# Kernel tuning notes

Measured on AMD Instinct MI355X. Metric: run time of the kernel, lower is better.

Reference implementation:

```python
import jax, jax.numpy as jnp
import numpy as np

N = 50000      # nodes
E = 800000     # edges
IN = 16        # embedding_dimension
HID = 128      # hidden_dimension
OUT = 3        # out_dim
R = 2          # relation_num
NEG_SLOPE = 0.2  # PyG RGATConv default negative_slope


def setup_inputs() -> dict:
    key = jax.random.key(0)
    ks = jax.random.split(key, 9)
    feature = jax.random.normal(ks[0], (N, IN), jnp.float32)
    edge_index = jax.random.randint(ks[1], (2, E), 0, N, jnp.int32)
    edge_type = jax.random.randint(ks[2], (E,), 0, R, jnp.int32)
    # RGATConv params (heads=1): weight [R, in, out], q/k [out, 1], bias [out]
    W1 = jax.random.normal(ks[3], (R, IN, HID), jnp.float32) * (1.0 / np.sqrt(IN))
    q1 = jax.random.normal(ks[4], (HID, 1), jnp.float32) * (1.0 / np.sqrt(HID))
    k1 = jax.random.normal(ks[5], (HID, 1), jnp.float32) * (1.0 / np.sqrt(HID))
    b1 = jnp.zeros((HID,), jnp.float32)
    W2 = jax.random.normal(ks[6], (R, HID, OUT), jnp.float32) * (1.0 / np.sqrt(HID))
    q2 = jax.random.normal(ks[7], (OUT, 1), jnp.float32) * (1.0 / np.sqrt(OUT))
    k2 = jax.random.normal(ks[8], (OUT, 1), jnp.float32) * (1.0 / np.sqrt(OUT))
    b2 = jnp.zeros((OUT,), jnp.float32)
    return dict(feature=feature, edge_index=edge_index, edge_type=edge_type,
                W1=W1, q1=q1, k1=k1, b1=b1, W2=W2, q2=q2, k2=k2, b2=b2)


def rgat_conv(x, src, dst, edge_type, W, q, k, b, n_nodes):
    # Per-relation node transform once at node level: [R, N, C]
    # (equivalent to per-edge bmm with W[edge_type] in PyG, but avoids
    #  gathering [E, in, C] weight matrices)
    xr = jnp.einsum('nd,rdc->rnc', x, W)
    out_i = xr[edge_type, dst]  # target node transformed by edge relation, [E, C]
    out_j = xr[edge_type, src]  # source node transformed by edge relation, [E, C]
    # additive self-attention, heads=1: alpha = leaky_relu(q(x_i) + k(x_j))
    alpha = jax.nn.leaky_relu((out_i @ q + out_j @ k)[:, 0], NEG_SLOPE)  # [E]
    # across-relation softmax over incoming edges of each target node
    m = jax.ops.segment_max(alpha, dst, num_segments=n_nodes)
    ex = jnp.exp(alpha - m[dst])
    denom = jax.ops.segment_sum(ex, dst, num_segments=n_nodes)
    a = ex / (denom[dst] + 1e-16)
    # message = alpha * W_r x_j, scatter-sum to target nodes
    out = jax.ops.segment_sum(out_j * a[:, None], dst, num_segments=n_nodes)
    return out + b


def reference(feature, edge_index, edge_type, W1, q1, k1, b1, W2, q2, k2, b2):
    src, dst = edge_index[0], edge_index[1]  # PyG: row 0 = source j, row 1 = target i
    h = rgat_conv(feature, src, dst, edge_type, W1, q1, k1, b1, N)
    # F.dropout(p=0.3) is identity in eval mode
    out = rgat_conv(h, src, dst, edge_type, W2, q2, k2, b2, N)
    return out
```

## Files before the change

### kernel.cpp

```cpp
#include <hip/hip_runtime.h>
#include <math.h>

#define IN_DIM 16
#define HID 128
#define NEG 0.2f
#define ABLK 8192
#define CAP 4608

__device__ __forceinline__ float lrelu(float a) { return a > 0.f ? a : NEG * a; }

__global__ void __launch_bounds__(256) k_pre(
    const float* __restrict__ W1, const float* __restrict__ q1, const float* __restrict__ k1,
    const float* __restrict__ b1, const float* __restrict__ W2, const float* __restrict__ q2,
    const float* __restrict__ k2,
    float* __restrict__ wq1, float* __restrict__ wk1,
    float* __restrict__ M, float* __restrict__ C,
    int* __restrict__ gCursor, int nbkt) {
    int zi = blockIdx.x * 256 + threadIdx.x;
    if (zi < nbkt) gCursor[zi] = 0;

    int w = blockIdx.x * 4 + (threadIdx.x >> 6);
    if (w >= 362) return;
    int lane = threadIdx.x & 63;

    auto T = [&](int c, int o) -> float {
        if (o < 3) return W2[c * 3 + o];
        if (o < 6) return W2[384 + c * 3 + (o - 3)];
        const float* base = (o == 6 || o == 8) ? (W2 + c * 3) : (W2 + 384 + c * 3);
        const float* v = (o < 8) ? q2 : k2;
        return base[0] * v[0] + base[1] * v[1] + base[2] * v[2];
    };

    if (w < 330) {
        bool isC = (w >= 320);
        int o  = isC ? (w - 320) : (w % 10);
        int dp = isC ? 0 : (w / 10);
        float acc = 0.f;
        for (int c = lane; c < HID; c += 64) {
            float left = isC ? b1[c] : W1[dp * HID + c];
            acc += left * T(c, o);
        }
#pragma unroll
        for (int off = 32; off; off >>= 1) acc += __shfl_xor(acc, off);
        if (lane == 0) { if (isC) C[o] = acc; else M[dp * 10 + o] = acc; }
    } else {
        int i = w - 330;
        float aq = 0.f, ak = 0.f;
        for (int c = lane; c < HID; c += 64) {
            float wv = W1[i * HID + c];
            aq += wv * q1[c]; ak += wv * k1[c];
        }
#pragma unroll
        for (int off = 32; off; off >>= 1) { aq += __shfl_xor(aq, off); ak += __shfl_xor(ak, off); }
        if (lane == 0) { wq1[i] = aq; wk1[i] = ak; }
    }
}

__global__ void __launch_bounds__(256) k_bin(
    const int* __restrict__ srcp, const int* __restrict__ dstp,
    const int* __restrict__ etp,
    int* __restrict__ gCursor, int* __restrict__ binned,
    const float* __restrict__ x,
    const float* __restrict__ wq1, const float* __restrict__ wk1,
    float* __restrict__ sq1, float* __restrict__ sk1,
    int n_nodes, int ecnt, int nbkt) {
    __shared__ int lh[256];
    __shared__ int runB[256];
    __shared__ float wq[2 * IN_DIM], wk[2 * IN_DIM];
    int t = threadIdx.x;
    lh[t] = 0;
    if (t < 2 * IN_DIM) { wq[t] = wq1[t]; wk[t] = wk1[t]; }
    __syncthreads();
    int E0 = blockIdx.x * ABLK;
    int rb[ABLK / 256];
#pragma unroll
    for (int k = 0; k < ABLK / 256; ++k) {
        int e = E0 + k * 256 + t;
        int v = -1;
        if (e < ecnt) {
            int b = dstp[e] >> 8;
            int r = atomicAdd(&lh[b], 1);
            v = (r << 8) | b;
        }
        rb[k] = v;
    }
    __syncthreads();
    if (t < nbkt && lh[t]) runB[t] = atomicAdd(&gCursor[t], lh[t]);
    __syncthreads();
#pragma unroll
    for (int k = 0; k < ABLK / 256; ++k) {
        int v = rb[k];
        if (v < 0) continue;
        int b = v & 255, r = v >> 8;
        int e = E0 + k * 256 + t;
        binned[b * CAP + runB[b] + r] = ((dstp[e] & 255) << 17) | (etp[e] << 16) | srcp[e];
    }
    int stride = gridDim.x * 256;
    for (int n = blockIdx.x * 256 + t; n < n_nodes; n += stride) {
        float q0 = 0.f, q1v = 0.f, k0 = 0.f, k1v = 0.f;
        const float4* xp = reinterpret_cast<const float4*>(x + (size_t)n * IN_DIM);
#pragma unroll
        for (int d4 = 0; d4 < IN_DIM / 4; ++d4) {
            float4 v = xp[d4];
            float vv[4] = {v.x, v.y, v.z, v.w};
#pragma unroll
            for (int j = 0; j < 4; ++j) {
                int d = d4 * 4 + j;
                q0 += vv[j] * wq[d]; q1v += vv[j] * wq[IN_DIM + d];
                k0 += vv[j] * wk[d]; k1v += vv[j] * wk[IN_DIM + d];
            }
        }
        sq1[n] = q0; sq1[n_nodes + n] = q1v;
        sk1[n] = k0; sk1[n_nodes + n] = k1v;
    }
}

__global__ void __launch_bounds__(256) k_build(
    const int* __restrict__ gCursor, const int* __restrict__ binned,
    int* __restrict__ offsets, int* __restrict__ sorted,
    int n_nodes, int ecnt, int nbkt) {
    __shared__ int ss[256], lh[256], loff[256], lcur[256];
    int t = threadIdx.x, b = blockIdx.x;
    int gv = (t < nbkt) ? gCursor[t] : 0;
    ss[t] = gv;
    lh[t] = 0;
    __syncthreads();
    for (int off = 1; off < 256; off <<= 1) {
        int u = (t >= off) ? ss[t - off] : 0;
        __syncthreads();
        ss[t] += u;
        __syncthreads();
    }
    int sz = gCursor[b];
    int myStart = ss[b] - sz;
    __syncthreads();
    for (int i = t; i < sz; i += 256) {
        int v = binned[b * CAP + i];
        atomicAdd(&lh[(v >> 17) & 255], 1);
    }
    __syncthreads();
    ss[t] = lh[t];
    __syncthreads();
    for (int off = 1; off < 256; off <<= 1) {
        int u = (t >= off) ? ss[t - off] : 0;
        __syncthreads();
        ss[t] += u;
        __syncthreads();
    }
    loff[t] = ss[t] - lh[t];
    lcur[t] = 0;
    __syncthreads();
    int node = b * 256 + t;
    if (node < n_nodes) offsets[node] = myStart + loff[t];
    if (b == nbkt - 1 && t == 0) offsets[n_nodes] = ecnt;
    for (int i = t; i < sz; i += 256) {
        int v = binned[b * CAP + i];
        int dl = (v >> 17) & 255;
        int p = loff[dl] + atomicAdd(&lcur[dl], 1);
        sorted[myStart + p] = v & 0x1FFFF;
    }
}

__global__ void __launch_bounds__(256) k_layer1(
    const int* __restrict__ offsets, const int* __restrict__ sorted,
    const float* __restrict__ sq1, const float* __restrict__ sk1,
    const float* __restrict__ x, const float* __restrict__ M, const float* __restrict__ C,
    float* __restrict__ xr2p, float* __restrict__ sq2,
    int n_nodes) {
    __shared__ float Ml[320], Cl[10];
    __shared__ float Al[4][32];
    for (int i = threadIdx.x; i < 320; i += 256) Ml[i] = M[i];
    if (threadIdx.x < 10)  Cl[threadIdx.x] = C[threadIdx.x];
    __syncthreads();
    int wid = threadIdx.x >> 6, lane = threadIdx.x & 63;
    int n = blockIdx.x * 4 + wid;
    if (n >= n_nodes) return;
    int beg = offsets[n], end = offsets[n + 1];
    float s0 = sq1[n], s1 = sq1[n_nodes + n];
    int ch4 = lane & 3, j = lane >> 2;
    float4 a0 = make_float4(0.f, 0.f, 0.f, 0.f);
    float4 a1 = make_float4(0.f, 0.f, 0.f, 0.f);
    float ds = 0.f;
    const float4* x4 = reinterpret_cast<const float4*>(x);
    for (int e = beg + j; e < end; e += 16) {
        int pk = sorted[e];
        int et = pk >> 16, s = pk & 0xFFFF;
        float w = __expf(lrelu((et ? s1 : s0) + sk1[et * n_nodes + s]));
        ds += w;
        float4 xv = x4[s * 4 + ch4];
        if (et == 0) { a0.x += w * xv.x; a0.y += w * xv.y; a0.z += w * xv.z; a0.w += w * xv.w; }
        else         { a1.x += w * xv.x; a1.y += w * xv.y; a1.z += w * xv.z; a1.w += w * xv.w; }
    }
#pragma unroll
    for (int off = 4; off <= 32; off <<= 1) {
        a0.x += __shfl_xor(a0.x, off); a0.y += __shfl_xor(a0.y, off);
        a0.z += __shfl_xor(a0.z, off); a0.w += __shfl_xor(a0.w, off);
        a1.x += __shfl_xor(a1.x, off); a1.y += __shfl_xor(a1.y, off);
        a1.z += __shfl_xor(a1.z, off); a1.w += __shfl_xor(a1.w, off);
        ds += __shfl_xor(ds, off);
    }
    float inv = 1.f / (ds + 1e-16f);
    if (lane < 4) {
        reinterpret_cast<float4*>(&Al[wid][0])[lane] =
            make_float4(a0.x * inv, a0.y * inv, a0.z * inv, a0.w * inv);
        reinterpret_cast<float4*>(&Al[wid][16])[lane] =
            make_float4(a1.x * inv, a1.y * inv, a1.z * inv, a1.w * inv);
    }
    if (lane < 10) {
        float acc = Cl[lane];
#pragma unroll
        for (int dp = 0; dp < 32; ++dp) acc += Al[wid][dp] * Ml[dp * 10 + lane];
        int o = lane;
        if (o < 3)       xr2p[(size_t)n * 4 + o] = acc;
        else if (o < 6)  xr2p[((size_t)n_nodes + n) * 4 + (o - 3)] = acc;
        else if (o == 6) sq2[2 * n] = acc;
        else if (o == 7) sq2[2 * n + 1] = acc;
        else if (o == 8) xr2p[(size_t)n * 4 + 3] = acc;
        else             xr2p[((size_t)n_nodes + n) * 4 + 3] = acc;
    }
}

__global__ void __launch_bounds__(256) k_node2(
    const int* __restrict__ offsets, const int* __restrict__ sorted,
    const float* __restrict__ sq2, const float* __restrict__ xr2p,
    const float* __restrict__ b2, float* __restrict__ out,
    int n_nodes) {
    int gid = blockIdx.x * 256 + threadIdx.x;
    int n = gid >> 4;
    int l = threadIdx.x & 15;
    if (n >= n_nodes) return;
    int beg = offsets[n], end = offsets[n + 1];
    if (beg == end) {
        if (l < 3) out[(size_t)n * 3 + l] = b2[l];
        return;
    }
    const float2 sq = *reinterpret_cast<const float2*>(sq2 + 2 * n);
    float lsum = 0.f, a0 = 0.f, a1 = 0.f, a2 = 0.f;
    for (int e = beg + l; e < end; e += 16) {
        int pk = sorted[e];
        int et = pk >> 16, s = pk & 0xFFFF;
        const float4 xr = *reinterpret_cast<const float4*>(xr2p + ((size_t)et * n_nodes + s) * 4);
        float w = __expf(lrelu((et ? sq.y : sq.x) + xr.w));
        lsum += w;
        a0 += w * xr.x; a1 += w * xr.y; a2 += w * xr.z;
    }
#pragma unroll
    for (int off = 8; off; off >>= 1) {
        lsum += __shfl_xor(lsum, off);
        a0 += __shfl_xor(a0, off);
        a1 += __shfl_xor(a1, off);
        a2 += __shfl_xor(a2, off);
    }
    if (l == 0) {
        float inv = 1.f / (lsum + 1e-16f);
        out[(size_t)n * 3 + 0] = a0 * inv + b2[0];
        out[(size_t)n * 3 + 1] = a1 * inv + b2[1];
        out[(size_t)n * 3 + 2] = a2 * inv + b2[2];
    }
}

extern "C" void kernel_launch(void* const* d_in, const int* in_sizes, int n_in,
                              void* d_out, int out_size, void* d_ws, size_t ws_size,
                              hipStream_t stream) {
    const float* x  = (const float*)d_in[0];
    const int*   ei = (const int*)d_in[1];
    const int*   etp = (const int*)d_in[2];
    const float* W1 = (const float*)d_in[3];
    const float* q1 = (const float*)d_in[4];
    const float* k1 = (const float*)d_in[5];
    const float* b1 = (const float*)d_in[6];
    const float* W2 = (const float*)d_in[7];
    const float* q2 = (const float*)d_in[8];
    const float* k2 = (const float*)d_in[9];
    const float* b2 = (const float*)d_in[10];
    float* out = (float*)d_out;

    const int n_nodes = in_sizes[0] / IN_DIM;
    const int ecnt    = in_sizes[2];
    const int* srcp = ei;
    const int* dstp = ei + ecnt;
    const int nbkt = (n_nodes + 255) >> 8;

    char* wp = (char*)d_ws;
    auto alloc = [&](size_t bytes) -> char* {
        char* p = wp;
        wp += (bytes + 255) & ~(size_t)255;
        return p;
    };
    float* xr2p  = (float*)alloc((size_t)2 * n_nodes * 4 * 4);
    float* sq1   = (float*)alloc((size_t)2 * n_nodes * 4);
    float* sk1   = (float*)alloc((size_t)2 * n_nodes * 4);
    float* sq2   = (float*)alloc((size_t)2 * n_nodes * 4);
    float* wq1   = (float*)alloc(32 * 4);
    float* wk1   = (float*)alloc(32 * 4);
    float* Mbuf  = (float*)alloc(320 * 4);
    float* Cbuf  = (float*)alloc(10 * 4);
    int* gCursor = (int*)alloc(256 * 4);
    int* offsets = (int*)alloc((size_t)(n_nodes + 1) * 4);
    int* binned  = (int*)alloc((size_t)nbkt * CAP * 4);
    int* sorted  = (int*)alloc((size_t)ecnt * 4);

    int nAblk = (ecnt + ABLK - 1) / ABLK;

    k_pre<<<91, 256, 0, stream>>>(W1, q1, k1, b1, W2, q2, k2, wq1, wk1, Mbuf, Cbuf,
                                  gCursor, nbkt);
    k_bin<<<nAblk, 256, 0, stream>>>(srcp, dstp, etp, gCursor, binned,
                                     x, wq1, wk1, sq1, sk1, n_nodes, ecnt, nbkt);
    k_build<<<nbkt, 256, 0, stream>>>(gCursor, binned, offsets, sorted, n_nodes, ecnt, nbkt);

    k_layer1<<<(n_nodes + 3) / 4, 256, 0, stream>>>(offsets, sorted, sq1, sk1, x, Mbuf, Cbuf,
                                                    xr2p, sq2, n_nodes);
    k_node2<<<(n_nodes * 16 + 255) / 256, 256, 0, stream>>>(offsets, sorted, sq2, xr2p, b2,
                                                            out, n_nodes);
}
```

Measured before the change: 93.39 us.

## Drop CSR build; aggregate per-bucket edges with shared-memory atomics

Removes the k_build counting-sort pass and the offsets/sorted arrays. Both layers now aggregate directly from the per-bucket binned edge lists, one 1024-thread block per 256-node bucket, and accumulate into shared-memory arrays with atomics. Layer 1 also applies the 16x10 projection matrix M per edge before accumulating, so it stores 11 accumulators per node instead of 32 features. This saves a kernel launch and a global scatter pass, at the cost of shared-atomic contention, more per-edge arithmetic, and only about 196 blocks, which is low parallelism.

```diff
diff --git a/kernel.cpp b/kernel.cpp
--- a/kernel.cpp
+++ b/kernel.cpp
@@ -115,147 +115,100 @@
     }
 }
 
-__global__ void __launch_bounds__(256) k_build(
+__global__ void __launch_bounds__(1024) k_agg1(
     const int* __restrict__ gCursor, const int* __restrict__ binned,
-    int* __restrict__ offsets, int* __restrict__ sorted,
-    int n_nodes, int ecnt, int nbkt) {
-    __shared__ int ss[256], lh[256], loff[256], lcur[256];
-    int t = threadIdx.x, b = blockIdx.x;
-    int gv = (t < nbkt) ? gCursor[t] : 0;
-    ss[t] = gv;
-    lh[t] = 0;
-    __syncthreads();
-    for (int off = 1; off < 256; off <<= 1) {
-        int u = (t >= off) ? ss[t - off] : 0;
-        __syncthreads();
-        ss[t] += u;
-        __syncthreads();
-    }
-    int sz = gCursor[b];
-    int myStart = ss[b] - sz;
-    __syncthreads();
-    for (int i = t; i < sz; i += 256) {
-        int v = binned[b * CAP + i];
-        atomicAdd(&lh[(v >> 17) & 255], 1);
-    }
-    __syncthreads();
-    ss[t] = lh[t];
-    __syncthreads();
-    for (int off = 1; off < 256; off <<= 1) {
-        int u = (t >= off) ? ss[t - off] : 0;
-        __syncthreads();
-        ss[t] += u;
-        __syncthreads();
-    }
-    loff[t] = ss[t] - lh[t];
-    lcur[t] = 0;
-    __syncthreads();
-    int node = b * 256 + t;
-    if (node < n_nodes) offsets[node] = myStart + loff[t];
-    if (b == nbkt - 1 && t == 0) offsets[n_nodes] = ecnt;
-    for (int i = t; i < sz; i += 256) {
-        int v = binned[b * CAP + i];
-        int dl = (v >> 17) & 255;
-        int p = loff[dl] + atomicAdd(&lcur[dl], 1);
-        sorted[myStart + p] = v & 0x1FFFF;
-    }
-}
-
-__global__ void __launch_bounds__(256) k_layer1(
-    const int* __restrict__ offsets, const int* __restrict__ sorted,
     const float* __restrict__ sq1, const float* __restrict__ sk1,
     const float* __restrict__ x, const float* __restrict__ M, const float* __restrict__ C,
-    float* __restrict__ xr2p, float* __restrict__ sq2,
-    int n_nodes) {
+    float* __restrict__ xr2p, float* __restrict__ sq2, int n_nodes) {
     __shared__ float Ml[320], Cl[10];
-    __shared__ float Al[4][32];
-    for (int i = threadIdx.x; i < 320; i += 256) Ml[i] = M[i];
-    if (threadIdx.x < 10)  Cl[threadIdx.x] = C[threadIdx.x];
-    __syncthreads();
-    int wid = threadIdx.x >> 6, lane = threadIdx.x & 63;
-    int n = blockIdx.x * 4 + wid;
-    if (n >= n_nodes) return;
-    int beg = offsets[n], end = offsets[n + 1];
-    float s0 = sq1[n], s1 = sq1[n_nodes + n];
-    int ch4 = lane & 3, j = lane >> 2;
-    float4 a0 = make_float4(0.f, 0.f, 0.f, 0.f);
-    float4 a1 = make_float4(0.f, 0.f, 0.f, 0.f);
-    float ds = 0.f;
+    __shared__ float sql[2][256];
+    __shared__ float acc[256][13];
+    int t = threadIdx.x, b = blockIdx.x;
+    for (int i = t; i < 320; i += 1024) Ml[i] = M[i];
+    if (t < 10) Cl[t] = C[t];
+    int nbase = b << 8;
+    if (t < 512) {
+        int r = t >> 8, dl = t & 255;
+        int n = nbase + dl;
+        sql[r][dl] = (n < n_nodes) ? sq1[r * n_nodes + n] : 0.f;
+    }
+    for (int i = t; i < 256 * 13; i += 1024) (&acc[0][0])[i] = 0.f;
+    __syncthreads();
+    int sz = gCursor[b];
     const float4* x4 = reinterpret_cast<const float4*>(x);
-    for (int e = beg + j; e < end; e += 16) {
-        int pk = sorted[e];
-        int et = pk >> 16, s = pk & 0xFFFF;
-        float w = __expf(lrelu((et ? s1 : s0) + sk1[et * n_nodes + s]));
-        ds += w;
-        float4 xv = x4[s * 4 + ch4];
-        if (et == 0) { a0.x += w * xv.x; a0.y += w * xv.y; a0.z += w * xv.z; a0.w += w * xv.w; }
-        else         { a1.x += w * xv.x; a1.y += w * xv.y; a1.z += w * xv.z; a1.w += w * xv.w; }
-    }
-#pragma unroll
-    for (int off = 4; off <= 32; off <<= 1) {
-        a0.x += __shfl_xor(a0.x, off); a0.y += __shfl_xor(a0.y, off);
-        a0.z += __shfl_xor(a0.z, off); a0.w += __shfl_xor(a0.w, off);
-        a1.x += __shfl_xor(a1.x, off); a1.y += __shfl_xor(a1.y, off);
-        a1.z += __shfl_xor(a1.z, off); a1.w += __shfl_xor(a1.w, off);
-        ds += __shfl_xor(ds, off);
-    }
-    float inv = 1.f / (ds + 1e-16f);
-    if (lane < 4) {
-        reinterpret_cast<float4*>(&Al[wid][0])[lane] =
-            make_float4(a0.x * inv, a0.y * inv, a0.z * inv, a0.w * inv);
-        reinterpret_cast<float4*>(&Al[wid][16])[lane] =
-            make_float4(a1.x * inv, a1.y * inv, a1.z * inv, a1.w * inv);
-    }
-    if (lane < 10) {
-        float acc = Cl[lane];
-#pragma unroll
-        for (int dp = 0; dp < 32; ++dp) acc += Al[wid][dp] * Ml[dp * 10 + lane];
-        int o = lane;
-        if (o < 3)       xr2p[(size_t)n * 4 + o] = acc;
-        else if (o < 6)  xr2p[((size_t)n_nodes + n) * 4 + (o - 3)] = acc;
-        else if (o == 6) sq2[2 * n] = acc;
-        else if (o == 7) sq2[2 * n + 1] = acc;
-        else if (o == 8) xr2p[(size_t)n * 4 + 3] = acc;
-        else             xr2p[((size_t)n_nodes + n) * 4 + 3] = acc;
-    }
-}
-
-__global__ void __launch_bounds__(256) k_node2(
-    const int* __restrict__ offsets, const int* __restrict__ sorted,
+    for (int i = t; i < sz; i += 1024) {
+        int v = binned[b * CAP + i];
+        int dl = (v >> 17) & 255, et = (v >> 16) & 1, s = v & 0xFFFF;
+        float w = __expf(lrelu(sql[et][dl] + sk1[et * n_nodes + s]));
+        float4 xa = x4[s * 4 + 0], xb = x4[s * 4 + 1];
+        float4 xc = x4[s * 4 + 2], xd = x4[s * 4 + 3];
+        float xv[16] = {xa.x, xa.y, xa.z, xa.w, xb.x, xb.y, xb.z, xb.w,
+                        xc.x, xc.y, xc.z, xc.w, xd.x, xd.y, xd.z, xd.w};
+        const float* Mr = &Ml[et * 160];
+        float* ab = acc[dl];
+#pragma unroll
+        for (int o = 0; o < 10; ++o) {
+            float a = 0.f;
+#pragma unroll
+            for (int dd = 0; dd < 16; ++dd) a += xv[dd] * Mr[dd * 10 + o];
+            atomicAdd(&ab[o], w * a);
+        }
+        atomicAdd(&ab[10], w);
+    }
+    __syncthreads();
+    if (t < 256) {
+        int n = nbase + t;
+        if (n < n_nodes) {
+            float inv = 1.f / (acc[t][10] + 1e-16f);
+            float o[10];
+#pragma unroll
+            for (int i = 0; i < 10; ++i) o[i] = acc[t][i] * inv + Cl[i];
+            reinterpret_cast<float4*>(xr2p)[n]           = make_float4(o[0], o[1], o[2], o[8]);
+            reinterpret_cast<float4*>(xr2p)[n_nodes + n] = make_float4(o[3], o[4], o[5], o[9]);
+            reinterpret_cast<float2*>(sq2)[n]            = make_float2(o[6], o[7]);
+        }
+    }
+}
+
+__global__ void __launch_bounds__(1024) k_agg2(
+    const int* __restrict__ gCursor, const int* __restrict__ binned,
     const float* __restrict__ sq2, const float* __restrict__ xr2p,
-    const float* __restrict__ b2, float* __restrict__ out,
-    int n_nodes) {
-    int gid = blockIdx.x * 256 + threadIdx.x;
-    int n = gid >> 4;
-    int l = threadIdx.x & 15;
-    if (n >= n_nodes) return;
-    int beg = offsets[n], end = offsets[n + 1];
-    if (beg == end) {
-        if (l < 3) out[(size_t)n * 3 + l] = b2[l];
-        return;
-    }
-    const float2 sq = *reinterpret_cast<const float2*>(sq2 + 2 * n);
-    float lsum = 0.f, a0 = 0.f, a1 = 0.f, a2 = 0.f;
-    for (int e = beg + l; e < end; e += 16) {
-        int pk = sorted[e];
-        int et = pk >> 16, s = pk & 0xFFFF;
-        const float4 xr = *reinterpret_cast<const float4*>(xr2p + ((size_t)et * n_nodes + s) * 4);
-        float w = __expf(lrelu((et ? sq.y : sq.x) + xr.w));
-        lsum += w;
-        a0 += w * xr.x; a1 += w * xr.y; a2 += w * xr.z;
-    }
-#pragma unroll
-    for (int off = 8; off; off >>= 1) {
-        lsum += __shfl_xor(lsum, off);
-        a0 += __shfl_xor(a0, off);
-        a1 += __shfl_xor(a1, off);
-        a2 += __shfl_xor(a2, off);
-    }
-    if (l == 0) {
-        float inv = 1.f / (lsum + 1e-16f);
-        out[(size_t)n * 3 + 0] = a0 * inv + b2[0];
-        out[(size_t)n * 3 + 1] = a1 * inv + b2[1];
-        out[(size_t)n * 3 + 2] = a2 * inv + b2[2];
+    const float* __restrict__ b2, float* __restrict__ out, int n_nodes) {
+    __shared__ float sql[256][2];
+    __shared__ float acc[256][5];
+    __shared__ float b2l[3];
+    int t = threadIdx.x, b = blockIdx.x;
+    if (t < 3) b2l[t] = b2[t];
+    int nbase = b << 8;
+    if (t < 256) {
+        int n = nbase + t;
+        float2 s = (n < n_nodes) ? reinterpret_cast<const float2*>(sq2)[n]
+                                 : make_float2(0.f, 0.f);
+        sql[t][0] = s.x; sql[t][1] = s.y;
+        acc[t][0] = acc[t][1] = acc[t][2] = acc[t][3] = 0.f;
+    }
+    __syncthreads();
+    int sz = gCursor[b];
+    for (int i = t; i < sz; i += 1024) {
+        int v = binned[b * CAP + i];
+        int dl = (v >> 17) & 255, et = (v >> 16) & 1, s = v & 0xFFFF;
+        float4 xr = reinterpret_cast<const float4*>(xr2p)[(size_t)et * n_nodes + s];
+        float w = __expf(lrelu(sql[dl][et] + xr.w));
+        float* ab = acc[dl];
+        atomicAdd(&ab[0], w * xr.x);
+        atomicAdd(&ab[1], w * xr.y);
+        atomicAdd(&ab[2], w * xr.z);
+        atomicAdd(&ab[3], w);
+    }
+    __syncthreads();
+    if (t < 256) {
+        int n = nbase + t;
+        if (n < n_nodes) {
+            float inv = 1.f / (acc[t][3] + 1e-16f);
+            out[(size_t)n * 3 + 0] = acc[t][0] * inv + b2l[0];
+            out[(size_t)n * 3 + 1] = acc[t][1] * inv + b2l[1];
+            out[(size_t)n * 3 + 2] = acc[t][2] * inv + b2l[2];
+        }
     }
 }
 
@@ -296,9 +249,7 @@
     float* Mbuf  = (float*)alloc(320 * 4);
     float* Cbuf  = (float*)alloc(10 * 4);
     int* gCursor = (int*)alloc(256 * 4);
-    int* offsets = (int*)alloc((size_t)(n_nodes + 1) * 4);
     int* binned  = (int*)alloc((size_t)nbkt * CAP * 4);
-    int* sorted  = (int*)alloc((size_t)ecnt * 4);
 
     int nAblk = (ecnt + ABLK - 1) / ABLK;
 
@@ -306,10 +257,7 @@
                                   gCursor, nbkt);
     k_bin<<<nAblk, 256, 0, stream>>>(srcp, dstp, etp, gCursor, binned,
                                      x, wq1, wk1, sq1, sk1, n_nodes, ecnt, nbkt);
-    k_build<<<nbkt, 256, 0, stream>>>(gCursor, binned, offsets, sorted, n_nodes, ecnt, nbkt);
-
-    k_layer1<<<(n_nodes + 3) / 4, 256, 0, stream>>>(offsets, sorted, sq1, sk1, x, Mbuf, Cbuf,
-                                                    xr2p, sq2, n_nodes);
-    k_node2<<<(n_nodes * 16 + 255) / 256, 256, 0, stream>>>(offsets, sorted, sq2, xr2p, b2,
-                                                            out, n_nodes);
-}
+    k_agg1<<<nbkt, 1024, 0, stream>>>(gCursor, binned, sq1, sk1, x, Mbuf, Cbuf,
+                                      xr2p, sq2, n_nodes);
+    k_agg2<<<nbkt, 1024, 0, stream>>>(gCursor, binned, sq2, xr2p, b2, out, n_nodes);
+}
```

Result: slower. 131.3 us (+40.6%).

## Fuse CSR build into layer kernels using per-bucket shared-memory sort

Applied to the files above, without the earlier changes.

Removes the separate k_build kernel and the global offsets/sorted arrays. Each layer kernel now runs one 1024-thread block per 256-node bucket, counting-sorts that bucket's binned edges into shared memory, then processes its nodes from LDS. This saves a kernel launch and the global write and read-back of the sorted edge list. In exchange the sort is done twice (once per layer), only 196 blocks are launched on a large GPU, and each block uses a lot of LDS, which may hurt parallelism and latency hiding.

```diff
diff --git a/kernel.cpp b/kernel.cpp
--- a/kernel.cpp
+++ b/kernel.cpp
@@ -115,147 +115,157 @@
     }
 }
 
-__global__ void __launch_bounds__(256) k_build(
+__global__ void __launch_bounds__(1024) k_l1(
     const int* __restrict__ gCursor, const int* __restrict__ binned,
-    int* __restrict__ offsets, int* __restrict__ sorted,
-    int n_nodes, int ecnt, int nbkt) {
-    __shared__ int ss[256], lh[256], loff[256], lcur[256];
+    const float* __restrict__ sq1, const float* __restrict__ sk1,
+    const float* __restrict__ x, const float* __restrict__ M, const float* __restrict__ C,
+    float* __restrict__ xr2p, float* __restrict__ sq2, int n_nodes) {
+    __shared__ float Ml[320], Cl[10];
+    __shared__ int lh[256], loff[256], lcur[256], ss[256];
+    __shared__ int sortedL[CAP];
+    __shared__ float Al[16][32];
     int t = threadIdx.x, b = blockIdx.x;
-    int gv = (t < nbkt) ? gCursor[t] : 0;
-    ss[t] = gv;
-    lh[t] = 0;
+    int nbase = b << 8;
+    for (int i = t; i < 320; i += 1024) Ml[i] = M[i];
+    if (t < 10) Cl[t] = C[t];
+    if (t < 256) { lh[t] = 0; lcur[t] = 0; }
+    __syncthreads();
+    int sz = gCursor[b];
+    for (int i = t; i < sz; i += 1024)
+        atomicAdd(&lh[(binned[b * CAP + i] >> 17) & 255], 1);
+    __syncthreads();
+    if (t < 256) ss[t] = lh[t];
     __syncthreads();
     for (int off = 1; off < 256; off <<= 1) {
-        int u = (t >= off) ? ss[t - off] : 0;
+        int u = (t >= off && t < 256) ? ss[t - off] : 0;
         __syncthreads();
-        ss[t] += u;
+        if (t < 256) ss[t] += u;
         __syncthreads();
     }
-    int sz = gCursor[b];
-    int myStart = ss[b] - sz;
-    __syncthreads();
-    for (int i = t; i < sz; i += 256) {
-        int v = binned[b * CAP + i];
-        atomicAdd(&lh[(v >> 17) & 255], 1);
-    }
-    __syncthreads();
-    ss[t] = lh[t];
-    __syncthreads();
-    for (int off = 1; off < 256; off <<= 1) {
-        int u = (t >= off) ? ss[t - off] : 0;
-        __syncthreads();
-        ss[t] += u;
-        __syncthreads();
-    }
-    loff[t] = ss[t] - lh[t];
-    lcur[t] = 0;
-    __syncthreads();
-    int node = b * 256 + t;
-    if (node < n_nodes) offsets[node] = myStart + loff[t];
-    if (b == nbkt - 1 && t == 0) offsets[n_nodes] = ecnt;
-    for (int i = t; i < sz; i += 256) {
+    if (t < 256) loff[t] = ss[t] - lh[t];
+    __syncthreads();
+    for (int i = t; i < sz; i += 1024) {
         int v = binned[b * CAP + i];
         int dl = (v >> 17) & 255;
         int p = loff[dl] + atomicAdd(&lcur[dl], 1);
-        sorted[myStart + p] = v & 0x1FFFF;
-    }
-}
-
-__global__ void __launch_bounds__(256) k_layer1(
-    const int* __restrict__ offsets, const int* __restrict__ sorted,
-    const float* __restrict__ sq1, const float* __restrict__ sk1,
-    const float* __restrict__ x, const float* __restrict__ M, const float* __restrict__ C,
-    float* __restrict__ xr2p, float* __restrict__ sq2,
-    int n_nodes) {
-    __shared__ float Ml[320], Cl[10];
-    __shared__ float Al[4][32];
-    for (int i = threadIdx.x; i < 320; i += 256) Ml[i] = M[i];
-    if (threadIdx.x < 10)  Cl[threadIdx.x] = C[threadIdx.x];
-    __syncthreads();
-    int wid = threadIdx.x >> 6, lane = threadIdx.x & 63;
-    int n = blockIdx.x * 4 + wid;
-    if (n >= n_nodes) return;
-    int beg = offsets[n], end = offsets[n + 1];
-    float s0 = sq1[n], s1 = sq1[n_nodes + n];
+        sortedL[p] = v & 0x1FFFF;
+    }
+    __syncthreads();
+    int wid = t >> 6, lane = t & 63;
     int ch4 = lane & 3, j = lane >> 2;
-    float4 a0 = make_float4(0.f, 0.f, 0.f, 0.f);
-    float4 a1 = make_float4(0.f, 0.f, 0.f, 0.f);
-    float ds = 0.f;
     const float4* x4 = reinterpret_cast<const float4*>(x);
-    for (int e = beg + j; e < end; e += 16) {
-        int pk = sorted[e];
-        int et = pk >> 16, s = pk & 0xFFFF;
-        float w = __expf(lrelu((et ? s1 : s0) + sk1[et * n_nodes + s]));
-        ds += w;
-        float4 xv = x4[s * 4 + ch4];
-        if (et == 0) { a0.x += w * xv.x; a0.y += w * xv.y; a0.z += w * xv.z; a0.w += w * xv.w; }
-        else         { a1.x += w * xv.x; a1.y += w * xv.y; a1.z += w * xv.z; a1.w += w * xv.w; }
-    }
-#pragma unroll
-    for (int off = 4; off <= 32; off <<= 1) {
-        a0.x += __shfl_xor(a0.x, off); a0.y += __shfl_xor(a0.y, off);
-        a0.z += __shfl_xor(a0.z, off); a0.w += __shfl_xor(a0.w, off);
-        a1.x += __shfl_xor(a1.x, off); a1.y += __shfl_xor(a1.y, off);
-        a1.z += __shfl_xor(a1.z, off); a1.w += __shfl_xor(a1.w, off);
-        ds += __shfl_xor(ds, off);
-    }
-    float inv = 1.f / (ds + 1e-16f);
-    if (lane < 4) {
-        reinterpret_cast<float4*>(&Al[wid][0])[lane] =
-            make_float4(a0.x * inv, a0.y * inv, a0.z * inv, a0.w * inv);
-        reinterpret_cast<float4*>(&Al[wid][16])[lane] =
-            make_float4(a1.x * inv, a1.y * inv, a1.z * inv, a1.w * inv);
-    }
-    if (lane < 10) {
-        float acc = Cl[lane];
-#pragma unroll
-        for (int dp = 0; dp < 32; ++dp) acc += Al[wid][dp] * Ml[dp * 10 + lane];
-        int o = lane;
-        if (o < 3)       xr2p[(size_t)n * 4 + o] = acc;
-        else if (o < 6)  xr2p[((size_t)n_nodes + n) * 4 + (o - 3)] = acc;
-        else if (o == 6) sq2[2 * n] = acc;
-        else if (o == 7) sq2[2 * n + 1] = acc;
-        else if (o == 8) xr2p[(size_t)n * 4 + 3] = acc;
-        else             xr2p[((size_t)n_nodes + n) * 4 + 3] = acc;
-    }
-}
-
-__global__ void __launch_bounds__(256) k_node2(
-    const int* __restrict__ offsets, const int* __restrict__ sorted,
+    for (int g = 0; g < 16; ++g) {
+        int dl = wid * 16 + g;
+        int n = nbase + dl;
+        if (n >= n_nodes) continue;
+        int beg = loff[dl], end = beg + lh[dl];
+        float s0 = sq1[n], s1 = sq1[n_nodes + n];
+        float4 a0 = make_float4(0.f, 0.f, 0.f, 0.f);
+        float4 a1 = make_float4(0.f, 0.f, 0.f, 0.f);
+        float ds = 0.f;
+        for (int e = beg + j; e < end; e += 16) {
+            int pk = sortedL[e];
+            int et = pk >> 16, s = pk & 0xFFFF;
+            float w = __expf(lrelu((et ? s1 : s0) + sk1[et * n_nodes + s]));
+            ds += w;
+            float4 xv = x4[s * 4 + ch4];
+            if (et == 0) { a0.x += w * xv.x; a0.y += w * xv.y; a0.z += w * xv.z; a0.w += w * xv.w; }
+            else         { a1.x += w * xv.x; a1.y += w * xv.y; a1.z += w * xv.z; a1.w += w * xv.w; }
+        }
+#pragma unroll
+        for (int off = 4; off <= 32; off <<= 1) {
+            a0.x += __shfl_xor(a0.x, off); a0.y += __shfl_xor(a0.y, off);
+            a0.z += __shfl_xor(a0.z, off); a0.w += __shfl_xor(a0.w, off);
+            a1.x += __shfl_xor(a1.x, off); a1.y += __shfl_xor(a1.y, off);
+            a1.z += __shfl_xor(a1.z, off); a1.w += __shfl_xor(a1.w, off);
+            ds += __shfl_xor(ds, off);
+        }
+        float inv = 1.f / (ds + 1e-16f);
+        if (lane < 4) {
+            reinterpret_cast<float4*>(&Al[wid][0])[lane] =
+                make_float4(a0.x * inv, a0.y * inv, a0.z * inv, a0.w * inv);
+            reinterpret_cast<float4*>(&Al[wid][16])[lane] =
+                make_float4(a1.x * inv, a1.y * inv, a1.z * inv, a1.w * inv);
+        }
+        if (lane < 10) {
+            float acc = Cl[lane];
+#pragma unroll
+            for (int dp = 0; dp < 32; ++dp) acc += Al[wid][dp] * Ml[dp * 10 + lane];
+            int o = lane;
+            if (o < 3)       xr2p[(size_t)n * 4 + o] = acc;
+            else if (o < 6)  xr2p[((size_t)n_nodes + n) * 4 + (o - 3)] = acc;
+            else if (o == 6) sq2[2 * n] = acc;
+            else if (o == 7) sq2[2 * n + 1] = acc;
+            else if (o == 8) xr2p[(size_t)n * 4 + 3] = acc;
+            else             xr2p[((size_t)n_nodes + n) * 4 + 3] = acc;
+        }
+    }
+}
+
+__global__ void __launch_bounds__(1024) k_l2(
+    const int* __restrict__ gCursor, const int* __restrict__ binned,
     const float* __restrict__ sq2, const float* __restrict__ xr2p,
-    const float* __restrict__ b2, float* __restrict__ out,
-    int n_nodes) {
-    int gid = blockIdx.x * 256 + threadIdx.x;
-    int n = gid >> 4;
-    int l = threadIdx.x & 15;
-    if (n >= n_nodes) return;
-    int beg = offsets[n], end = offsets[n + 1];
-    if (beg == end) {
-        if (l < 3) out[(size_t)n * 3 + l] = b2[l];
-        return;
-    }
-    const float2 sq = *reinterpret_cast<const float2*>(sq2 + 2 * n);
-    float lsum = 0.f, a0 = 0.f, a1 = 0.f, a2 = 0.f;
-    for (int e = beg + l; e < end; e += 16) {
-        int pk = sorted[e];
-        int et = pk >> 16, s = pk & 0xFFFF;
-        const float4 xr = *reinterpret_cast<const float4*>(xr2p + ((size_t)et * n_nodes + s) * 4);
-        float w = __expf(lrelu((et ? sq.y : sq.x) + xr.w));
-        lsum += w;
-        a0 += w * xr.x; a1 += w * xr.y; a2 += w * xr.z;
-    }
-#pragma unroll
-    for (int off = 8; off; off >>= 1) {
-        lsum += __shfl_xor(lsum, off);
-        a0 += __shfl_xor(a0, off);
-        a1 += __shfl_xor(a1, off);
-        a2 += __shfl_xor(a2, off);
-    }
-    if (l == 0) {
-        float inv = 1.f / (lsum + 1e-16f);
-        out[(size_t)n * 3 + 0] = a0 * inv + b2[0];
-        out[(size_t)n * 3 + 1] = a1 * inv + b2[1];
-        out[(size_t)n * 3 + 2] = a2 * inv + b2[2];
+    const float* __restrict__ b2, float* __restrict__ out, int n_nodes) {
+    __shared__ int lh[256], loff[256], lcur[256], ss[256];
+    __shared__ int sortedL[CAP];
+    __shared__ float b2l[3];
+    int t = threadIdx.x, b = blockIdx.x;
+    int nbase = b << 8;
+    if (t < 3) b2l[t] = b2[t];
+    if (t < 256) { lh[t] = 0; lcur[t] = 0; }
+    __syncthreads();
+    int sz = gCursor[b];
+    for (int i = t; i < sz; i += 1024)
+        atomicAdd(&lh[(binned[b * CAP + i] >> 17) & 255], 1);
+    __syncthreads();
+    if (t < 256) ss[t] = lh[t];
+    __syncthreads();
+    for (int off = 1; off < 256; off <<= 1) {
+        int u = (t >= off && t < 256) ? ss[t - off] : 0;
+        __syncthreads();
+        if (t < 256) ss[t] += u;
+        __syncthreads();
+    }
+    if (t < 256) loff[t] = ss[t] - lh[t];
+    __syncthreads();
+    for (int i = t; i < sz; i += 1024) {
+        int v = binned[b * CAP + i];
+        int dl = (v >> 17) & 255;
+        int p = loff[dl] + atomicAdd(&lcur[dl], 1);
+        sortedL[p] = v & 0x1FFFF;
+    }
+    __syncthreads();
+    int wid = t >> 6, lane = t & 63;
+    int l = lane & 15;
+    const float4* xr4 = reinterpret_cast<const float4*>(xr2p);
+    for (int g = 0; g < 4; ++g) {
+        int dl = wid * 16 + g * 4 + (lane >> 4);
+        int n = nbase + dl;
+        bool valid = (n < n_nodes);
+        int beg = loff[dl], end = beg + lh[dl];
+        float2 sq = valid ? reinterpret_cast<const float2*>(sq2)[n] : make_float2(0.f, 0.f);
+        float lsum = 0.f, a0 = 0.f, a1 = 0.f, a2 = 0.f;
+        for (int e = beg + l; e < end; e += 16) {
+            int pk = sortedL[e];
+            int et = pk >> 16, s = pk & 0xFFFF;
+            float4 xr = xr4[(size_t)et * n_nodes + s];
+            float w = __expf(lrelu((et ? sq.y : sq.x) + xr.w));
+            lsum += w;
+            a0 += w * xr.x; a1 += w * xr.y; a2 += w * xr.z;
+        }
+#pragma unroll
+        for (int off = 8; off; off >>= 1) {
+            lsum += __shfl_xor(lsum, off);
+            a0 += __shfl_xor(a0, off);
+            a1 += __shfl_xor(a1, off);
+            a2 += __shfl_xor(a2, off);
+        }
+        if (l == 0 && valid) {
+            float inv = 1.f / (lsum + 1e-16f);
+            out[(size_t)n * 3 + 0] = a0 * inv + b2l[0];
+            out[(size_t)n * 3 + 1] = a1 * inv + b2l[1];
+            out[(size_t)n * 3 + 2] = a2 * inv + b2l[2];
+        }
     }
 }
 
@@ -296,9 +306,7 @@
     float* Mbuf  = (float*)alloc(320 * 4);
     float* Cbuf  = (float*)alloc(10 * 4);
     int* gCursor = (int*)alloc(256 * 4);
-    int* offsets = (int*)alloc((size_t)(n_nodes + 1) * 4);
     int* binned  = (int*)alloc((size_t)nbkt * CAP * 4);
-    int* sorted  = (int*)alloc((size_t)ecnt * 4);
 
     int nAblk = (ecnt + ABLK - 1) / ABLK;
 
@@ -306,10 +314,7 @@
                                   gCursor, nbkt);
     k_bin<<<nAblk, 256, 0, stream>>>(srcp, dstp, etp, gCursor, binned,
                                      x, wq1, wk1, sq1, sk1, n_nodes, ecnt, nbkt);
-    k_build<<<nbkt, 256, 0, stream>>>(gCursor, binned, offsets, sorted, n_nodes, ecnt, nbkt);
-
-    k_layer1<<<(n_nodes + 3) / 4, 256, 0, stream>>>(offsets, sorted, sq1, sk1, x, Mbuf, Cbuf,
-                                                    xr2p, sq2, n_nodes);
-    k_node2<<<(n_nodes * 16 + 255) / 256, 256, 0, stream>>>(offsets, sorted, sq2, xr2p, b2,
-                                                            out, n_nodes);
-}
+    k_l1<<<nbkt, 1024, 0, stream>>>(gCursor, binned, sq1, sk1, x, Mbuf, Cbuf,
+                                    xr2p, sq2, n_nodes);
+    k_l2<<<nbkt, 1024, 0, stream>>>(gCursor, binned, sq2, xr2p, b2, out, n_nodes);
+}
```

Result: slower. 97.63 us (+4.5%).
